# Kernel tuning notes

Hardware: AMD Instinct MI355X
Metric: run time of the kernel (lower is better)

## Reference

```python
import jax, jax.numpy as jnp
import numpy as np

B, A, C, M = 8, 120000, 9, 64
ALPHA, GAMMA = 0.25, 2.0


def setup_inputs() -> dict:
    key = jax.random.key(0)
    k1, k2, k3, k4, k5, k6, k7 = jax.random.split(key, 7)
    # anchors: plausible rotated boxes [x1,y1,x2,y2,angle]
    cx = jax.random.uniform(k1, (A,), minval=0.0, maxval=1024.0)
    cy = jax.random.uniform(k2, (A,), minval=0.0, maxval=1024.0)
    w = jax.random.uniform(k3, (A,), minval=16.0, maxval=128.0)
    h = jax.random.uniform(k4, (A,), minval=16.0, maxval=128.0)
    ang = jax.random.uniform(k5, (A,), minval=0.0, maxval=np.pi)
    anchor = jnp.stack([cx - 0.5 * w, cy - 0.5 * h, cx + 0.5 * w, cy + 0.5 * h, ang], axis=1)
    anchors = anchor[None]  # [1, A, 5]
    # annotations: copies of distinct anchor boxes -> guaranteed IoU=1 matches
    idx = jnp.arange(B * M).reshape(B, M)  # disjoint anchor indices per image
    boxes = anchor[idx]  # [B, M, 5]
    cls_col = jax.random.randint(k6, (B, M), 1, 4).astype(jnp.float32)  # class in {1,2,3} < C
    flag = jnp.zeros((B, M, 1), jnp.float32)  # valid (!= -1)
    annotations = jnp.concatenate([boxes[..., :4], cls_col[..., None], flag], axis=-1)  # [B, M, 6]
    classifications = jax.random.uniform(k7, (B, A, C), minval=0.0, maxval=1.0)
    regressions = jax.random.normal(jax.random.fold_in(key, 9), (B, A, 5)) * 0.1
    return {
        "classifications": classifications,
        "regressions": regressions,
        "anchors": anchors,
        "annotations": annotations,
    }


def _per_image(cls_p, reg, ann, anchor):
    # cls_p: [A,C], reg: [A,5], ann: [M,6], anchor: [A,5]
    valid = ann[:, 5] != -1.0
    has_ann = jnp.any(valid)
    p = jnp.clip(cls_p, 1e-4, 1.0 - 1e-4)
    a, b = anchor, ann[:, :5]
    # pairwise rotated IoU (arIoU)  [A, M]
    iw = jnp.clip(jnp.minimum(a[:, 2, None], b[None, :, 2]) - jnp.maximum(a[:, 0, None], b[None, :, 0]), 0.0)
    ih = jnp.clip(jnp.minimum(a[:, 3, None], b[None, :, 3]) - jnp.maximum(a[:, 1, None], b[None, :, 1]), 0.0)
    area_a = (a[:, 2] - a[:, 0]) * (a[:, 3] - a[:, 1])
    area_b = (b[:, 2] - b[:, 0]) * (b[:, 3] - b[:, 1])
    inter = iw * ih
    ua = jnp.clip(area_a[:, None] + area_b[None, :] - inter, 1e-8)
    iou = inter / ua
    ariou = iou * jnp.cos(jnp.abs(a[:, 4, None] - b[None, :, 4]) - np.pi / 2)
    ariou = jnp.where(valid[None, :], ariou, -1e9)  # mask invalid annotations
    iou_max = ariou.max(axis=1)
    iou_arg = ariou.argmax(axis=1)
    assigned = ann[iou_arg]  # [A, 6]
    pos = iou_max >= 0.5
    neg = iou_max < 0.4
    num_pos = pos.sum().astype(p.dtype)
    # targets: -1 = ignore, one-hot for positives, 0 for negatives
    cls_idx = assigned[:, 4].astype(jnp.int32)
    onehot = jax.nn.one_hot(cls_idx, p.shape[1], dtype=p.dtype)
    targets = jnp.where(pos[:, None], onehot, jnp.where(neg[:, None], 0.0, -1.0))
    # focal BCE
    alpha_factor = jnp.where(targets == 1.0, ALPHA, 1.0 - ALPHA)
    focal_weight = alpha_factor * jnp.where(targets == 1.0, 1.0 - p, p) ** GAMMA
    ce = -(targets * jnp.log(p) + (1.0 - targets) * jnp.log(1.0 - p))
    cls_loss = jnp.where(targets != -1.0, focal_weight * ce, 0.0).sum() / jnp.maximum(num_pos, 1.0)
    aw = a[:, 2] - a[:, 0]
    ah = a[:, 3] - a[:, 1]
    acx = a[:, 0] + 0.5 * aw
    acy = a[:, 1] + 0.5 * ah
    gw_raw = assigned[:, 2] - assigned[:, 0]
    gh_raw = assigned[:, 3] - assigned[:, 1]
    gcx = assigned[:, 0] + 0.5 * gw_raw
    gcy = assigned[:, 1] + 0.5 * gh_raw
    gw = jnp.clip(gw_raw, 1.0)
    gh = jnp.clip(gh_raw, 1.0)
    t = jnp.stack(
        [(gcx - acx) / aw, (gcy - acy) / ah, jnp.log(gw / aw), jnp.log(gh / ah), jnp.tan(assigned[:, 4] - a[:, 4])],
        axis=1,
    ) / jnp.array([[0.1, 0.1, 0.2, 0.2, 1.0]], dtype=p.dtype)
    diff = jnp.abs(t - reg)
    sl1 = jnp.where(diff <= 1.0 / 9.0, 0.5 * 9.0 * diff * diff, diff - 0.5 / 9.0)
    reg_loss = jnp.where(num_pos > 0.0, (sl1 * pos[:, None]).sum() / jnp.maximum(num_pos * 5.0, 1.0), 0.0)
    cls_loss = jnp.where(has_ann, cls_loss, 0.0)
    reg_loss = jnp.where(has_ann, reg_loss, 0.0)
    return cls_loss, reg_loss


def reference(classifications, regressions, anchors, annotations):
    anchor = anchors[0]
    cls_l, reg_l = jax.vmap(_per_image, in_axes=(0, 0, 0, None))(classifications, regressions, annotations, anchor)
    return cls_l.mean(keepdims=True), reg_l.mean(keepdims=True)
```

## Files before the change

kernel.cpp:

```cpp
#include <hip/hip_runtime.h>
#include <math.h>


constexpr int Bn = 8, An = 120000, Cn = 9, Mn = 64;
constexpr int R = 4;
constexpr int TPB = 256;
constexpr int APB = TPB * R;
constexpr int GX = (An + APB - 1) / APB;

__global__ __launch_bounds__(TPB, 4) void focal_main(
    const float* __restrict__ cls,
    const float* __restrict__ reg,
    const float* __restrict__ anchors,
    const float* __restrict__ ann,
    float* __restrict__ ws)
{
    __shared__ float4 sT[Mn][2];
    __shared__ float sred[4][3];

    const int tid = threadIdx.x;
    const int b = blockIdx.y;
    const int base = blockIdx.x * APB + tid;

    if (tid < Mn) {
        const float* a6 = ann + ((size_t)b * Mn + tid) * 6;
        float x1 = a6[0], y1 = a6[1], x2 = a6[2], y2 = a6[3];
        float cv = a6[4], fl = a6[5];
        float sb, cb;
        sincosf(cv, &sb, &cb);
        if (fl == -1.0f) { x1 = y1 = x2 = y2 = 0.f; sb = cb = 0.f; cv = 0.f; }
        sT[tid][0] = make_float4(x1, y1, x2, y2);
        sT[tid][1] = make_float4(sb, cb, (x2 - x1) * (y2 - y1), cv);
    }
    __syncthreads();

    float ax1[R], ay1[R], ax2[R], ay2[R], areaA[R], sa[R], ca[R], aangv[R];
    float bestA[R], bestB[R];
    int bestK[R];
    bool act[R];

    #pragma unroll
    for (int r = 0; r < R; ++r) {
        const int i = base + r * TPB;
        act[r] = (i < An);
        bestA[r] = 0.f; bestB[r] = 1.f; bestK[r] = 0;
        if (act[r]) {
            const float* a5 = anchors + (size_t)i * 5;
            ax1[r] = a5[0]; ay1[r] = a5[1]; ax2[r] = a5[2]; ay2[r] = a5[3];
            aangv[r] = a5[4];
            areaA[r] = (ax2[r] - ax1[r]) * (ay2[r] - ay1[r]);
            sincosf(aangv[r], &sa[r], &ca[r]);
        } else {
            ax1[r] = ay1[r] = ax2[r] = ay2[r] = 0.f;
            areaA[r] = 0.f; sa[r] = 0.f; ca[r] = 0.f; aangv[r] = 0.f;
        }
    }

    #pragma unroll 4
    for (int k = 0; k < Mn; ++k) {
        const float4 bx = sT[k][0];
        const float4 au = sT[k][1];
        #pragma unroll
        for (int r = 0; r < R; ++r) {
            float iw = fminf(ax2[r], bx.z) - fmaxf(ax1[r], bx.x);
            float ih = fminf(ay2[r], bx.w) - fmaxf(ay1[r], bx.y);
            iw = fmaxf(iw, 0.f); ih = fmaxf(ih, 0.f);
            float inter = iw * ih;
            float ua = fmaxf(areaA[r] + au.z - inter, 1e-8f);
            float s = fabsf(sa[r] * au.y - ca[r] * au.x);
            float av = inter * s;
            bool upd = (av * bestB[r] > bestA[r] * ua);
            bestA[r] = upd ? av : bestA[r];
            bestB[r] = upd ? ua : bestB[r];
            bestK[r] = upd ? k : bestK[r];
        }
    }

    float csum = 0.f, rsum = 0.f, pcnt = 0.f;

    #pragma unroll
    for (int r = 0; r < R; ++r) {
        if (!act[r]) continue;
        const int i = base + r * TPB;
        const float iou = bestA[r] / bestB[r];
        const bool pos = iou >= 0.5f;
        const bool neg = iou < 0.4f;

        if (pos || neg) {
            const float4 au = sT[bestK[r]][1];
            const int ci = (int)au.w;
            const float* pc = cls + ((size_t)b * An + i) * (size_t)Cn;
            #pragma unroll
            for (int c = 0; c < Cn; ++c) {
                float p = fminf(fmaxf(pc[c], 1e-4f), 0.9999f);
                bool hit = pos && (c == ci);
                float t = hit ? (1.f - p) : p;
                float m = hit ? p : (1.f - p);
                float w = hit ? 0.25f : 0.75f;
                csum += w * t * t * (-__logf(m));
            }
        }

        if (pos) {
            pcnt += 1.f;
            const float4 gb = sT[bestK[r]][0];
            const float4 au = sT[bestK[r]][1];
            float aw = ax2[r] - ax1[r], ah = ay2[r] - ay1[r];
            float acx = ax1[r] + 0.5f * aw, acy = ay1[r] + 0.5f * ah;
            float gwr = gb.z - gb.x, ghr = gb.w - gb.y;
            float gcx = gb.x + 0.5f * gwr, gcy = gb.y + 0.5f * ghr;
            float gw = fmaxf(gwr, 1.f), gh = fmaxf(ghr, 1.f);
            float tt[5];
            tt[0] = ((gcx - acx) / aw) * 10.f;
            tt[1] = ((gcy - acy) / ah) * 10.f;
            tt[2] = logf(gw / aw) * 5.f;
            tt[3] = logf(gh / ah) * 5.f;
            tt[4] = tanf(au.w - aangv[r]);
            const float* rg = reg + ((size_t)b * An + i) * 5;
            #pragma unroll
            for (int j = 0; j < 5; ++j) {
                float d = fabsf(tt[j] - rg[j]);
                rsum += (d <= (1.f / 9.f)) ? (4.5f * d * d) : (d - (0.5f / 9.f));
            }
        }
    }

    #pragma unroll
    for (int off = 32; off > 0; off >>= 1) {
        csum += __shfl_down(csum, off, 64);
        rsum += __shfl_down(rsum, off, 64);
        pcnt += __shfl_down(pcnt, off, 64);
    }
    const int wave = tid >> 6;
    if ((tid & 63) == 0) {
        sred[wave][0] = csum; sred[wave][1] = rsum; sred[wave][2] = pcnt;
    }
    __syncthreads();
    if (tid == 0) {
        float c = sred[0][0] + sred[1][0] + sred[2][0] + sred[3][0];
        float r = sred[0][1] + sred[1][1] + sred[2][1] + sred[3][1];
        float p = sred[0][2] + sred[1][2] + sred[2][2] + sred[3][2];
        const int j = b * GX + blockIdx.x;
        ws[j * 4 + 0] = c;
        ws[j * 4 + 1] = r;
        ws[j * 4 + 2] = p;
    }
}

__global__ __launch_bounds__(512) void focal_final(
    const float* __restrict__ ann,
    const float* __restrict__ ws,
    float* __restrict__ out)
{
    __shared__ float simg[Bn][2];
    const int tid = threadIdx.x;
    const int w = tid >> 6;
    const int lane = tid & 63;

    float c = 0.f, r = 0.f, p = 0.f;
    for (int j = lane; j < GX; j += 64) {
        const int idx = (w * GX + j) * 4;
        c += ws[idx + 0]; r += ws[idx + 1]; p += ws[idx + 2];
    }
    float fl = ann[((size_t)w * Mn + lane) * 6 + 5];
    bool has = __any(fl != -1.0f);

    #pragma unroll
    for (int off = 32; off > 0; off >>= 1) {
        c += __shfl_down(c, off, 64);
        r += __shfl_down(r, off, 64);
        p += __shfl_down(p, off, 64);
    }
    if (lane == 0) {
        float cl = 0.f, rl = 0.f;
        if (has) {
            cl = c / fmaxf(p, 1.f);
            rl = (p > 0.f) ? r / fmaxf(p * 5.f, 1.f) : 0.f;
        }
        simg[w][0] = cl; simg[w][1] = rl;
    }
    __syncthreads();
    if (tid == 0) {
        float cl = 0.f, rl = 0.f;
        #pragma unroll
        for (int b = 0; b < Bn; ++b) { cl += simg[b][0]; rl += simg[b][1]; }
        out[0] = cl / (float)Bn;
        out[1] = rl / (float)Bn;
    }
}

extern "C" void kernel_launch(void* const* d_in, const int* in_sizes, int n_in,
                              void* d_out, int out_size, void* d_ws, size_t ws_size,
                              hipStream_t stream) {
    const float* cls     = (const float*)d_in[0];
    const float* reg     = (const float*)d_in[1];
    const float* anchors = (const float*)d_in[2];
    const float* ann     = (const float*)d_in[3];
    float* out = (float*)d_out;
    float* ws  = (float*)d_ws;

    dim3 grid(GX, Bn);
    focal_main<<<grid, TPB, 0, stream>>>(cls, reg, anchors, ann, ws);
    focal_final<<<1, 512, 0, stream>>>(ann, ws, out);
}
```

Baseline: 126.3 us.

## Use single-wave blocks, vectorize loads, and prefetch class scores before IoU loop

Shrinks blocks to one 64-thread wave, which removes the shared-memory cross-wave reduction and its barrier and makes every thread load one annotation. Anchor and annotation reads become unaligned vector loads. The nine class probabilities are loaded up front into registers so their latency overlaps the 64-annotation IoU loop, and the IoU division is replaced by cross-multiplied comparisons. The cost is more registers per thread and four times as many blocks, and every anchor now loads class scores even when it is ignored; the final reduction kernel reads GX entries per image, which grows with the smaller tile.

```diff
diff --git a/kernel.cpp b/kernel.cpp
--- a/kernel.cpp
+++ b/kernel.cpp
@@ -4,11 +4,14 @@
 
 constexpr int Bn = 8, An = 120000, Cn = 9, Mn = 64;
 constexpr int R = 4;
-constexpr int TPB = 256;
+constexpr int TPB = 64;
 constexpr int APB = TPB * R;
 constexpr int GX = (An + APB - 1) / APB;
 
-__global__ __launch_bounds__(TPB, 4) void focal_main(
+typedef float f4 __attribute__((ext_vector_type(4), aligned(4)));
+typedef float f2 __attribute__((ext_vector_type(2), aligned(4)));
+
+__global__ __launch_bounds__(TPB) void focal_main(
     const float* __restrict__ cls,
     const float* __restrict__ reg,
     const float* __restrict__ anchors,
@@ -16,19 +19,19 @@
     float* __restrict__ ws)
 {
     __shared__ float4 sT[Mn][2];
-    __shared__ float sred[4][3];
 
     const int tid = threadIdx.x;
     const int b = blockIdx.y;
     const int base = blockIdx.x * APB + tid;
 
-    if (tid < Mn) {
+    {
         const float* a6 = ann + ((size_t)b * Mn + tid) * 6;
-        float x1 = a6[0], y1 = a6[1], x2 = a6[2], y2 = a6[3];
-        float cv = a6[4], fl = a6[5];
+        f4 v0 = *(const f4*)a6;
+        f2 v1 = *(const f2*)(a6 + 4);
+        float x1 = v0.x, y1 = v0.y, x2 = v0.z, y2 = v0.w, cv = v1.x;
         float sb, cb;
         sincosf(cv, &sb, &cb);
-        if (fl == -1.0f) { x1 = y1 = x2 = y2 = 0.f; sb = cb = 0.f; cv = 0.f; }
+        if (v1.y == -1.0f) { x1 = y1 = x2 = y2 = 0.f; sb = cb = 0.f; cv = 0.f; }
         sT[tid][0] = make_float4(x1, y1, x2, y2);
         sT[tid][1] = make_float4(sb, cb, (x2 - x1) * (y2 - y1), cv);
     }
@@ -38,22 +41,25 @@
     float bestA[R], bestB[R];
     int bestK[R];
     bool act[R];
+    f4 c0[R], c1[R];
+    float c8[R];
 
     #pragma unroll
     for (int r = 0; r < R; ++r) {
         const int i = base + r * TPB;
         act[r] = (i < An);
+        const int ii = act[r] ? i : (An - 1);
         bestA[r] = 0.f; bestB[r] = 1.f; bestK[r] = 0;
-        if (act[r]) {
-            const float* a5 = anchors + (size_t)i * 5;
-            ax1[r] = a5[0]; ay1[r] = a5[1]; ax2[r] = a5[2]; ay2[r] = a5[3];
-            aangv[r] = a5[4];
-            areaA[r] = (ax2[r] - ax1[r]) * (ay2[r] - ay1[r]);
-            sincosf(aangv[r], &sa[r], &ca[r]);
-        } else {
-            ax1[r] = ay1[r] = ax2[r] = ay2[r] = 0.f;
-            areaA[r] = 0.f; sa[r] = 0.f; ca[r] = 0.f; aangv[r] = 0.f;
-        }
+        const float* a5 = anchors + (size_t)ii * 5;
+        f4 av5 = *(const f4*)a5;
+        ax1[r] = av5.x; ay1[r] = av5.y; ax2[r] = av5.z; ay2[r] = av5.w;
+        aangv[r] = a5[4];
+        areaA[r] = (ax2[r] - ax1[r]) * (ay2[r] - ay1[r]);
+        sincosf(aangv[r], &sa[r], &ca[r]);
+        const float* pc = cls + ((size_t)b * An + ii) * (size_t)Cn;
+        c0[r] = *(const f4*)pc;
+        c1[r] = *(const f4*)(pc + 4);
+        c8[r] = pc[8];
     }
 
     #pragma unroll 4
@@ -82,17 +88,17 @@
     for (int r = 0; r < R; ++r) {
         if (!act[r]) continue;
         const int i = base + r * TPB;
-        const float iou = bestA[r] / bestB[r];
-        const bool pos = iou >= 0.5f;
-        const bool neg = iou < 0.4f;
+        const bool pos = bestA[r] >= 0.5f * bestB[r];
+        const bool neg = bestA[r] <  0.4f * bestB[r];
 
         if (pos || neg) {
             const float4 au = sT[bestK[r]][1];
             const int ci = (int)au.w;
-            const float* pc = cls + ((size_t)b * An + i) * (size_t)Cn;
+            float pv[9] = { c0[r].x, c0[r].y, c0[r].z, c0[r].w,
+                            c1[r].x, c1[r].y, c1[r].z, c1[r].w, c8[r] };
             #pragma unroll
             for (int c = 0; c < Cn; ++c) {
-                float p = fminf(fmaxf(pc[c], 1e-4f), 0.9999f);
+                float p = fminf(fmaxf(pv[c], 1e-4f), 0.9999f);
                 bool hit = pos && (c == ci);
                 float t = hit ? (1.f - p) : p;
                 float m = hit ? p : (1.f - p);
@@ -131,19 +137,11 @@
         rsum += __shfl_down(rsum, off, 64);
         pcnt += __shfl_down(pcnt, off, 64);
     }
-    const int wave = tid >> 6;
-    if ((tid & 63) == 0) {
-        sred[wave][0] = csum; sred[wave][1] = rsum; sred[wave][2] = pcnt;
-    }
-    __syncthreads();
     if (tid == 0) {
-        float c = sred[0][0] + sred[1][0] + sred[2][0] + sred[3][0];
-        float r = sred[0][1] + sred[1][1] + sred[2][1] + sred[3][1];
-        float p = sred[0][2] + sred[1][2] + sred[2][2] + sred[3][2];
         const int j = b * GX + blockIdx.x;
-        ws[j * 4 + 0] = c;
-        ws[j * 4 + 1] = r;
-        ws[j * 4 + 2] = p;
+        ws[j * 4 + 0] = csum;
+        ws[j * 4 + 1] = rsum;
+        ws[j * 4 + 2] = pcnt;
     }
 }
 
```

After: 134.2 us. 6.2% more time.
